# Kernel tuning notes

Hardware: AMD Instinct MI355X
Metric: run time of the kernel (lower is better)

The kernel has to match this reference:

```python
import jax, jax.numpy as jnp
import numpy as np

ROPE_BASE = 10000.0

def _rope_cos_sin(T, d, dtype):
    inv_freq = 1.0 / (ROPE_BASE ** (jnp.arange(0, d, 2, dtype=jnp.float32) / d))
    t = jnp.arange(T, dtype=jnp.float32)
    freqs = t[:, None] * inv_freq[None, :]           # [T, d/2]
    emb = jnp.concatenate([freqs, freqs], axis=-1)   # [T, d]
    return jnp.cos(emb).astype(dtype), jnp.sin(emb).astype(dtype)

def _rotate_half(x):
    x1, x2 = jnp.split(x, 2, axis=-1)
    return jnp.concatenate([-x2, x1], axis=-1)

def setup_inputs() -> dict:
    key = jax.random.key(0)
    k1, k2, k3, k4 = jax.random.split(key, 4)
    B, T, C, H = 4, 4096, 1024, 64
    x = jax.random.normal(k1, (B, T, C), dtype=jnp.float32)
    s = 1.0 / np.sqrt(C)
    Wq = jax.random.normal(k2, (H, C), dtype=jnp.float32) * s
    Wk = jax.random.normal(k3, (H, C), dtype=jnp.float32) * s
    Wv = jax.random.normal(k4, (H, C), dtype=jnp.float32) * s
    return {"x": x, "Wq": Wq, "Wk": Wk, "Wv": Wv}

def reference(x, Wq, Wk, Wv):
    B, T, C = x.shape
    H = Wq.shape[0]
    q = jnp.einsum('btc,hc->bth', x, Wq)
    k = jnp.einsum('btc,hc->bth', x, Wk)
    v = jnp.einsum('btc,hc->bth', x, Wv)
    cos, sin = _rope_cos_sin(T, H, x.dtype)
    q = q * cos + _rotate_half(q) * sin
    k = k * cos + _rotate_half(k) * sin
    # NOTE: original scales by dim_model**-0.5 (C), not head_size
    wei = jnp.einsum('bth,bsh->bts', q, k) * (C ** -0.5)
    causal = jnp.tril(jnp.ones((T, T), dtype=bool))
    wei = jnp.where(causal, wei, -jnp.inf)
    wei = jax.nn.softmax(wei, axis=-1)
    # dropout p=0.0 (identity)
    out = jnp.einsum('bts,bsh->bth', wei, v)
    return out
```

## Files before the change

### kernel.cpp

```cpp
#include <hip/hip_runtime.h>
#include <hip/hip_bf16.h>
#include <math.h>

typedef __attribute__((ext_vector_type(8))) __bf16 bf16x8;
typedef __attribute__((ext_vector_type(4))) float f32x4;
typedef __attribute__((ext_vector_type(16))) float f32x16;
typedef __attribute__((ext_vector_type(4))) float float4_t;
typedef __attribute__((ext_vector_type(4))) unsigned int uint4_t;

#define NB 4
#define TSEQ 4096
#define CD 1024
#define HD 64
#define NCH 16
#define CHT 4
#define QB 32

static __device__ __forceinline__ unsigned short f2bf(float f) {
    union { float f; unsigned u; } v; v.f = f;
    unsigned r = v.u + 0x7fffu + ((v.u >> 16) & 1u);
    return (unsigned short)(r >> 16);
}
static __device__ __forceinline__ float bf2f(unsigned short u) {
    union { unsigned int i; float f; } v; v.i = ((unsigned int)u) << 16;
    return v.f;
}
static __device__ __forceinline__ unsigned int pk2(float a, float b) {
    union { __bf16 h[2]; unsigned int u; } x;
    x.h[0] = (__bf16)a; x.h[1] = (__bf16)b;
    return x.u;
}

__global__ __launch_bounds__(256) void wcvt_kernel(const float* __restrict__ wq,
                                                   const float* __restrict__ wk,
                                                   const float* __restrict__ wv,
                                                   unsigned short* __restrict__ wb) {
    int i = blockIdx.x * 256 + threadIdx.x;
    int j = i >> 10;
    int col = i & 1023;
    int jb = j >> 4, off = j & 15;
    int sub = ((jb & 1) << 5) | ((jb & 2) << 3);
    int srcrow = (jb < 8) ? (sub + off) : ((jb - 8) * 16 + off);
    const float* src = (jb < 4) ? wq : ((jb < 8) ? wk : wv);
    wb[i] = f2bf(src[srcrow * 1024 + col]);
}

__global__ __launch_bounds__(256) void qkv_kernel(const float* __restrict__ x,
                                                  const unsigned short* __restrict__ wb,
                                                  unsigned short* __restrict__ qo,
                                                  unsigned short* __restrict__ ko,
                                                  unsigned short* __restrict__ vt) {
    __shared__ unsigned short xs[64][72];
    __shared__ unsigned short ws[64][72];
    const int tid = threadIdx.x;
    const int wave = tid >> 6, lane = tid & 63;
    const int lr = lane & 15;
    const int lk = (lane >> 4) << 3;
    const int rowg = (lane >> 4) << 2;
    const int row0 = blockIdx.x * 64;
    const int cbi = blockIdx.y;
    const int cb = cbi * 64;

    f32x4 acc[4];
#pragma unroll
    for (int i = 0; i < 4; ++i) acc[i] = (f32x4){0.f, 0.f, 0.f, 0.f};

    const int sr = tid >> 2;
    const int sc = (tid & 3) << 4;

    for (int k0 = 0; k0 < CD; k0 += 64) {
        __syncthreads();
        {
            const float4_t* s4 =
                reinterpret_cast<const float4_t*>(x + (size_t)(row0 + sr) * CD + k0 + sc);
            alignas(16) unsigned short tmp[16];
#pragma unroll
            for (int j = 0; j < 4; ++j) {
                float4_t f = s4[j];
#pragma unroll
                for (int e = 0; e < 4; ++e) tmp[j * 4 + e] = f2bf(f[e]);
            }
            *reinterpret_cast<uint4_t*>(&xs[sr][sc]) = *reinterpret_cast<const uint4_t*>(&tmp[0]);
            *reinterpret_cast<uint4_t*>(&xs[sr][sc + 8]) = *reinterpret_cast<const uint4_t*>(&tmp[8]);
        }
        {
            const uint4_t* wsrc =
                reinterpret_cast<const uint4_t*>(wb + (size_t)(cb + sr) * CD + k0 + sc);
            *reinterpret_cast<uint4_t*>(&ws[sr][sc]) = wsrc[0];
            *reinterpret_cast<uint4_t*>(&ws[sr][sc + 8]) = wsrc[1];
        }
        __syncthreads();
#pragma unroll
        for (int kk = 0; kk < 2; ++kk) {
            bf16x8 a = *reinterpret_cast<const bf16x8*>(&xs[wave * 16 + lr][kk * 32 + lk]);
#pragma unroll
            for (int c = 0; c < 4; ++c) {
                bf16x8 bfr = *reinterpret_cast<const bf16x8*>(&ws[c * 16 + lr][kk * 32 + lk]);
                acc[c] = __builtin_amdgcn_mfma_f32_16x16x32_bf16(a, bfr, acc[c], 0, 0, 0);
            }
        }
    }

    const int gr0 = row0 + wave * 16 + rowg;
    const int bidx = gr0 >> 12;
    const int tb = gr0 & (TSEQ - 1);
    if (cbi < 2) {
        unsigned short* o = (cbi == 0) ? qo : ko;
        const float sc2 = (cbi == 0) ? 0.045084218764560315f : 1.0f;
        const float l2b = 0.4152410118609215f;
        const float invf0 = exp2f(-(float)lr * l2b);
        const float invf1 = exp2f(-(float)(lr + 16) * l2b);
#pragma unroll
        for (int r = 0; r < 4; ++r) {
            float t = (float)(tb + r);
            float s0, c0, s1, c1;
            sincosf(t * invf0, &s0, &c0);
            sincosf(t * invf1, &s1, &c1);
            size_t ro = (size_t)(gr0 + r) * HD;
            float lo, hi;
            lo = acc[0][r]; hi = acc[1][r];
            o[ro + 0 + lr]  = f2bf((lo * c0 - hi * s0) * sc2);
            o[ro + 32 + lr] = f2bf((hi * c0 + lo * s0) * sc2);
            lo = acc[2][r]; hi = acc[3][r];
            o[ro + 16 + lr] = f2bf((lo * c1 - hi * s1) * sc2);
            o[ro + 48 + lr] = f2bf((hi * c1 + lo * s1) * sc2);
        }
    } else {
#pragma unroll
        for (int r = 0; r < 4; ++r) {
            size_t vbase = (size_t)bidx * HD * TSEQ + (size_t)(tb + r);
            vt[vbase + (size_t)(0 + lr) * TSEQ]  = f2bf(acc[0][r]);
            vt[vbase + (size_t)(16 + lr) * TSEQ] = f2bf(acc[1][r]);
            vt[vbase + (size_t)(32 + lr) * TSEQ] = f2bf(acc[2][r]);
            vt[vbase + (size_t)(48 + lr) * TSEQ] = f2bf(acc[3][r]);
        }
    }
}

__global__ __launch_bounds__(256, 4) void attn_partial(const unsigned short* __restrict__ q,
                                                       const unsigned short* __restrict__ k,
                                                       const unsigned short* __restrict__ vt,
                                                       unsigned short* __restrict__ po,
                                                       float* __restrict__ pm,
                                                       float* __restrict__ pl) {
    const int chunk = blockIdx.x, qb = blockIdx.y, b = blockIdx.z;
    const int ktend_blk = 2 * qb + 1;
    const int kt0 = chunk * CHT;
    if (kt0 > ktend_blk) return;
    const int ktend = min(ktend_blk, kt0 + CHT - 1);

    __shared__ unsigned short ks[64][72];
    __shared__ unsigned short vs[64][72];
    const int tid = threadIdx.x;
    const int wave = tid >> 6, lane = tid & 63;
    const int l31 = lane & 31;
    const int h = lane >> 5;
    const int h8 = h << 3;
    const int qrow0 = qb * 128 + wave * 32;
    const int qpos = qrow0 + l31;

    const unsigned short* qb_ = q + ((size_t)(b * TSEQ + qpos)) * HD + h8;
    bf16x8 qf[4];
#pragma unroll
    for (int s = 0; s < 4; ++s)
        qf[s] = *reinterpret_cast<const bf16x8*>(qb_ + 16 * s);

    f32x16 oacc[2];
#pragma unroll
    for (int dt = 0; dt < 2; ++dt)
#pragma unroll
        for (int r = 0; r < 16; ++r) oacc[dt][r] = 0.f;
    float mreg = -1.0e30f;
    float lsum = 0.f;

    const int srow = tid >> 2;
    const int scol = (tid & 3) << 4;
    const unsigned short* kbase = k + (size_t)b * TSEQ * HD;
    const unsigned short* vbase = vt + (size_t)b * HD * TSEQ;
    uint4_t kr[2], vr[2];

    auto loadtile = [&](int kt) {
        const int s0l = kt * 64;
        const unsigned short* kp = kbase + (size_t)(s0l + srow) * HD + scol;
        const unsigned short* vp = vbase + (size_t)srow * TSEQ + s0l + scol;
        kr[0] = *reinterpret_cast<const uint4_t*>(kp);
        kr[1] = *reinterpret_cast<const uint4_t*>(kp + 8);
        vr[0] = *reinterpret_cast<const uint4_t*>(vp);
        vr[1] = *reinterpret_cast<const uint4_t*>(vp + 8);
    };

    loadtile(kt0);

    for (int kt = kt0; kt <= ktend; ++kt) {
        const int s0 = kt * 64;
        __syncthreads();
        *reinterpret_cast<uint4_t*>(&ks[srow][scol]) = kr[0];
        *reinterpret_cast<uint4_t*>(&ks[srow][scol + 8]) = kr[1];
        *reinterpret_cast<uint4_t*>(&vs[srow][scol]) = vr[0];
        *reinterpret_cast<uint4_t*>(&vs[srow][scol + 8]) = vr[1];
        __syncthreads();
        if (kt < ktend) loadtile(kt + 1);

        if (s0 > qrow0 + 31) continue;

        f32x16 sacc[2];
#pragma unroll
        for (int blk = 0; blk < 2; ++blk)
#pragma unroll
            for (int r = 0; r < 16; ++r) sacc[blk][r] = 0.f;
        __builtin_amdgcn_s_setprio(1);
#pragma unroll
        for (int s = 0; s < 4; ++s) {
            bf16x8 ka = *reinterpret_cast<const bf16x8*>(&ks[l31][16 * s + h8]);
            bf16x8 kb2 = *reinterpret_cast<const bf16x8*>(&ks[32 + l31][16 * s + h8]);
            sacc[0] = __builtin_amdgcn_mfma_f32_32x32x16_bf16(ka, qf[s], sacc[0], 0, 0, 0);
            sacc[1] = __builtin_amdgcn_mfma_f32_32x32x16_bf16(kb2, qf[s], sacc[1], 0, 0, 0);
        }
        __builtin_amdgcn_s_setprio(0);

        if (s0 + 63 > qrow0) {
#pragma unroll
            for (int blk = 0; blk < 2; ++blk)
#pragma unroll
                for (int r = 0; r < 16; ++r) {
                    int kvpos = s0 + 32 * blk + (r & 3) + ((r >> 2) << 3) + (h << 2);
                    if (kvpos > qpos) sacc[blk][r] = -INFINITY;
                }
        }

        float tm[8];
#pragma unroll
        for (int r = 0; r < 8; ++r)
            tm[r] = fmaxf(fmaxf(sacc[0][r], sacc[0][r + 8]),
                          fmaxf(sacc[1][r], sacc[1][r + 8]));
#pragma unroll
        for (int r = 0; r < 4; ++r) tm[r] = fmaxf(tm[r], tm[r + 4]);
        float mx = fmaxf(fmaxf(tm[0], tm[1]), fmaxf(tm[2], tm[3]));
        mx = fmaxf(mx, __shfl_xor(mx, 32, 64));

        const bool newmax = !__all(mx <= mreg + 7.0f);
        if (newmax) {
            float mnew = fmaxf(mreg, mx);
            float corr = __builtin_amdgcn_exp2f(mreg - mnew);
            mreg = mnew;
            lsum *= corr;
#pragma unroll
            for (int dt = 0; dt < 2; ++dt)
#pragma unroll
                for (int r = 0; r < 16; ++r) oacc[dt][r] *= corr;
        }

        float pvv[2][16];
#pragma unroll
        for (int blk = 0; blk < 2; ++blk)
#pragma unroll
            for (int r = 0; r < 16; ++r)
                pvv[blk][r] = __builtin_amdgcn_exp2f(sacc[blk][r] - mreg);
        float ts[8];
#pragma unroll
        for (int r = 0; r < 8; ++r)
            ts[r] = (pvv[0][r] + pvv[0][r + 8]) + (pvv[1][r] + pvv[1][r + 8]);
#pragma unroll
        for (int r = 0; r < 4; ++r) ts[r] += ts[r + 4];
        float psum = (ts[0] + ts[1]) + (ts[2] + ts[3]);
        psum += __shfl_xor(psum, 32, 64);
        lsum += psum;

        unsigned int cw[2][4][2];
#pragma unroll
        for (int blk = 0; blk < 2; ++blk)
#pragma unroll
            for (int G = 0; G < 4; ++G) {
                cw[blk][G][0] = pk2(pvv[blk][4 * G], pvv[blk][4 * G + 1]);
                cw[blk][G][1] = pk2(pvv[blk][4 * G + 2], pvv[blk][4 * G + 3]);
            }

        const bool hif = (h == 1);
        __builtin_amdgcn_s_setprio(1);
#pragma unroll
        for (int s = 0; s < 4; ++s) {
            const int blk = s >> 1, base = (s & 1) << 1;
            unsigned int a0 = cw[blk][base][0],     a1 = cw[blk][base][1];
            unsigned int b0 = cw[blk][base + 1][0], b1 = cw[blk][base + 1][1];
            unsigned int s0w = hif ? a0 : b0;
            unsigned int s1w = hif ? a1 : b1;
            unsigned int r0 = __shfl_xor(s0w, 32, 64);
            unsigned int r1 = __shfl_xor(s1w, 32, 64);
            uint4_t pw;
            pw[0] = hif ? r0 : a0;
            pw[1] = hif ? r1 : a1;
            pw[2] = hif ? b0 : r0;
            pw[3] = hif ? b1 : r1;
            bf16x8 pfrag = *reinterpret_cast<const bf16x8*>(&pw);
            bf16x8 v0 = *reinterpret_cast<const bf16x8*>(&vs[l31][16 * s + h8]);
            bf16x8 v1 = *reinterpret_cast<const bf16x8*>(&vs[32 + l31][16 * s + h8]);
            oacc[0] = __builtin_amdgcn_mfma_f32_32x32x16_bf16(v0, pfrag, oacc[0], 0, 0, 0);
            oacc[1] = __builtin_amdgcn_mfma_f32_32x32x16_bf16(v1, pfrag, oacc[1], 0, 0, 0);
        }
        __builtin_amdgcn_s_setprio(0);
    }

    const int slot = (((b << 5) + qb) << 4) + chunk;
    unsigned short* pob = po + (size_t)slot * 8192;
#pragma unroll
    for (int dt = 0; dt < 2; ++dt)
#pragma unroll
        for (int r = 0; r < 16; ++r) {
            int d = 32 * dt + (r & 3) + ((r >> 2) << 3) + (h << 2);
            pob[d * 128 + wave * 32 + l31] = f2bf(oacc[dt][r]);
        }
    if (h == 0) {
        pm[slot * 128 + wave * 32 + l31] = mreg;
        pl[slot * 128 + wave * 32 + l31] = lsum;
    }
}

__global__ __launch_bounds__(256) void attn_combine(const unsigned short* __restrict__ po,
                                                    const float* __restrict__ pm,
                                                    const float* __restrict__ pl,
                                                    float* __restrict__ out) {
    __shared__ float sm[64][17];
    const int bq = blockIdx.x;
    const int dg = blockIdx.y;
    const int qt = bq & 63;
    const int b = bq >> 6;
    const int qb = qt >> 1, half = qt & 1;
    const int nch = (qb >> 1) + 1;
    const int qi = threadIdx.x & 63;
    const int jj = threadIdx.x >> 6;
    const int slotb = (((b << 5) + qb) << 4);
    const int qoff = half * 64 + qi;

    float pmv[NCH];
#pragma unroll
    for (int c = 0; c < NCH; ++c)
        pmv[c] = (c < nch) ? pm[(size_t)(slotb + c) * 128 + qoff] : -1.0e30f;
    float tmv[NCH];
#pragma unroll
    for (int c = 0; c < NCH; ++c) tmv[c] = pmv[c];
#pragma unroll
    for (int s = NCH / 2; s >= 1; s >>= 1)
#pragma unroll
        for (int c = 0; c < NCH / 2; ++c)
            if (c < s) tmv[c] = fmaxf(tmv[c], tmv[c + s]);
    const float M = tmv[0];

    float L = 0.f;
    float a0 = 0.f, a1 = 0.f, a2 = 0.f, a3 = 0.f;
    const int dbase = dg * 16 + jj * 4;
#pragma unroll 4
    for (int c = 0; c < nch; ++c) {
        float w = exp2f(pmv[c] - M);
        L += w * pl[(size_t)(slotb + c) * 128 + qoff];
        const unsigned short* p = po + (size_t)(slotb + c) * 8192 + dbase * 128 + qoff;
        a0 += w * bf2f(p[0]);
        a1 += w * bf2f(p[128]);
        a2 += w * bf2f(p[256]);
        a3 += w * bf2f(p[384]);
    }
    const float inv = 1.f / L;
    sm[qi][jj * 4 + 0] = a0 * inv;
    sm[qi][jj * 4 + 1] = a1 * inv;
    sm[qi][jj * 4 + 2] = a2 * inv;
    sm[qi][jj * 4 + 3] = a3 * inv;
    __syncthreads();
    const int row = threadIdx.x >> 2;
    const int c4 = (threadIdx.x & 3) << 2;
    float4_t f;
#pragma unroll
    for (int e = 0; e < 4; ++e) f[e] = sm[row][c4 + e];
    *reinterpret_cast<float4_t*>(out + (size_t)bq * 4096 + row * 64 + dg * 16 + c4) = f;
}

extern "C" void kernel_launch(void* const* d_in, const int* in_sizes, int n_in,
                              void* d_out, int out_size, void* d_ws, size_t ws_size,
                              hipStream_t stream) {
    const float* x = (const float*)d_in[0];
    const float* wq = (const float*)d_in[1];
    const float* wk = (const float*)d_in[2];
    const float* wv = (const float*)d_in[3];
    float* out = (float*)d_out;

    unsigned short* wb = (unsigned short*)d_ws;
    unsigned short* qb = wb + 3 * HD * CD;
    unsigned short* kb = qb + (size_t)NB * TSEQ * HD;
    unsigned short* vtb = kb + (size_t)NB * TSEQ * HD;
    unsigned short* pob = vtb + (size_t)NB * TSEQ * HD;
    float* pm = (float*)(pob + (size_t)2048 * 8192);
    float* pl = pm + (size_t)2048 * 128;

    wcvt_kernel<<<768, 256, 0, stream>>>(wq, wk, wv, wb);
    qkv_kernel<<<dim3(256, 3), 256, 0, stream>>>(x, wb, qb, kb, vtb);
    attn_partial<<<dim3(NCH, QB, NB), 256, 0, stream>>>(qb, kb, vtb, pob, pm, pl);
    attn_combine<<<dim3(NB * 64, 4), 256, 0, stream>>>(pob, pm, pl, out);
}
```

Baseline: 63.29 us.

## Enlarge attention query block to 256 rows with 512-thread blocks

```diff
diff --git a/kernel.cpp b/kernel.cpp
--- a/kernel.cpp
+++ b/kernel.cpp
@@ -14,7 +14,7 @@
 #define HD 64
 #define NCH 16
 #define CHT 4
-#define QB 32
+#define QBL 16
 
 static __device__ __forceinline__ unsigned short f2bf(float f) {
     union { float f; unsigned u; } v; v.f = f;
@@ -73,15 +73,14 @@
         {
             const float4_t* s4 =
                 reinterpret_cast<const float4_t*>(x + (size_t)(row0 + sr) * CD + k0 + sc);
-            alignas(16) unsigned short tmp[16];
-#pragma unroll
-            for (int j = 0; j < 4; ++j) {
-                float4_t f = s4[j];
-#pragma unroll
-                for (int e = 0; e < 4; ++e) tmp[j * 4 + e] = f2bf(f[e]);
-            }
-            *reinterpret_cast<uint4_t*>(&xs[sr][sc]) = *reinterpret_cast<const uint4_t*>(&tmp[0]);
-            *reinterpret_cast<uint4_t*>(&xs[sr][sc + 8]) = *reinterpret_cast<const uint4_t*>(&tmp[8]);
+            float4_t f0 = s4[0], f1 = s4[1], f2 = s4[2], f3 = s4[3];
+            uint4_t w0, w1;
+            w0[0] = pk2(f0[0], f0[1]); w0[1] = pk2(f0[2], f0[3]);
+            w0[2] = pk2(f1[0], f1[1]); w0[3] = pk2(f1[2], f1[3]);
+            w1[0] = pk2(f2[0], f2[1]); w1[1] = pk2(f2[2], f2[3]);
+            w1[2] = pk2(f3[0], f3[1]); w1[3] = pk2(f3[2], f3[3]);
+            *reinterpret_cast<uint4_t*>(&xs[sr][sc]) = w0;
+            *reinterpret_cast<uint4_t*>(&xs[sr][sc + 8]) = w1;
         }
         {
             const uint4_t* wsrc =
@@ -137,14 +136,14 @@
     }
 }
 
-__global__ __launch_bounds__(256, 4) void attn_partial(const unsigned short* __restrict__ q,
+__global__ __launch_bounds__(512, 4) void attn_partial(const unsigned short* __restrict__ q,
                                                        const unsigned short* __restrict__ k,
                                                        const unsigned short* __restrict__ vt,
                                                        unsigned short* __restrict__ po,
                                                        float* __restrict__ pm,
                                                        float* __restrict__ pl) {
     const int chunk = blockIdx.x, qb = blockIdx.y, b = blockIdx.z;
-    const int ktend_blk = 2 * qb + 1;
+    const int ktend_blk = 4 * qb + 3;
     const int kt0 = chunk * CHT;
     if (kt0 > ktend_blk) return;
     const int ktend = min(ktend_blk, kt0 + CHT - 1);
@@ -156,7 +155,7 @@
     const int l31 = lane & 31;
     const int h = lane >> 5;
     const int h8 = h << 3;
-    const int qrow0 = qb * 128 + wave * 32;
+    const int qrow0 = qb * 256 + wave * 32;
     const int qpos = qrow0 + l31;
 
     const unsigned short* qb_ = q + ((size_t)(b * TSEQ + qpos)) * HD + h8;
@@ -173,20 +172,16 @@
     float mreg = -1.0e30f;
     float lsum = 0.f;
 
-    const int srow = tid >> 2;
-    const int scol = (tid & 3) << 4;
+    const int srow = tid >> 3;
+    const int scol = (tid & 7) << 3;
     const unsigned short* kbase = k + (size_t)b * TSEQ * HD;
     const unsigned short* vbase = vt + (size_t)b * HD * TSEQ;
-    uint4_t kr[2], vr[2];
+    uint4_t kr, vr;
 
     auto loadtile = [&](int kt) {
         const int s0l = kt * 64;
-        const unsigned short* kp = kbase + (size_t)(s0l + srow) * HD + scol;
-        const unsigned short* vp = vbase + (size_t)srow * TSEQ + s0l + scol;
-        kr[0] = *reinterpret_cast<const uint4_t*>(kp);
-        kr[1] = *reinterpret_cast<const uint4_t*>(kp + 8);
-        vr[0] = *reinterpret_cast<const uint4_t*>(vp);
-        vr[1] = *reinterpret_cast<const uint4_t*>(vp + 8);
+        kr = *reinterpret_cast<const uint4_t*>(kbase + (size_t)(s0l + srow) * HD + scol);
+        vr = *reinterpret_cast<const uint4_t*>(vbase + (size_t)srow * TSEQ + s0l + scol);
     };
 
     loadtile(kt0);
@@ -194,10 +189,8 @@
     for (int kt = kt0; kt <= ktend; ++kt) {
         const int s0 = kt * 64;
         __syncthreads();
-        *reinterpret_cast<uint4_t*>(&ks[srow][scol]) = kr[0];
-        *reinterpret_cast<uint4_t*>(&ks[srow][scol + 8]) = kr[1];
-        *reinterpret_cast<uint4_t*>(&vs[srow][scol]) = vr[0];
-        *reinterpret_cast<uint4_t*>(&vs[srow][scol + 8]) = vr[1];
+        *reinterpret_cast<uint4_t*>(&ks[srow][scol]) = kr;
+        *reinterpret_cast<uint4_t*>(&vs[srow][scol]) = vr;
         __syncthreads();
         if (kt < ktend) loadtile(kt + 1);
 
@@ -300,18 +293,18 @@
         __builtin_amdgcn_s_setprio(0);
     }
 
-    const int slot = (((b << 5) + qb) << 4) + chunk;
-    unsigned short* pob = po + (size_t)slot * 8192;
+    const int slot = (((b << 4) + qb) << 4) + chunk;
+    unsigned short* pob = po + (size_t)slot * 16384;
 #pragma unroll
     for (int dt = 0; dt < 2; ++dt)
 #pragma unroll
         for (int r = 0; r < 16; ++r) {
             int d = 32 * dt + (r & 3) + ((r >> 2) << 3) + (h << 2);
-            pob[d * 128 + wave * 32 + l31] = f2bf(oacc[dt][r]);
+            pob[d * 256 + wave * 32 + l31] = f2bf(oacc[dt][r]);
         }
     if (h == 0) {
-        pm[slot * 128 + wave * 32 + l31] = mreg;
-        pl[slot * 128 + wave * 32 + l31] = lsum;
+        pm[slot * 256 + wave * 32 + l31] = mreg;
+        pl[slot * 256 + wave * 32 + l31] = lsum;
     }
 }
 
@@ -324,17 +317,17 @@
     const int dg = blockIdx.y;
     const int qt = bq & 63;
     const int b = bq >> 6;
-    const int qb = qt >> 1, half = qt & 1;
-    const int nch = (qb >> 1) + 1;
+    const int qb = qt >> 2, quarter = qt & 3;
+    const int nch = qb + 1;
     const int qi = threadIdx.x & 63;
     const int jj = threadIdx.x >> 6;
-    const int slotb = (((b << 5) + qb) << 4);
-    const int qoff = half * 64 + qi;
+    const int slotb = (((b << 4) + qb) << 4);
+    const int qoff = quarter * 64 + qi;
 
     float pmv[NCH];
 #pragma unroll
     for (int c = 0; c < NCH; ++c)
-        pmv[c] = (c < nch) ? pm[(size_t)(slotb + c) * 128 + qoff] : -1.0e30f;
+        pmv[c] = (c < nch) ? pm[(size_t)(slotb + c) * 256 + qoff] : -1.0e30f;
     float tmv[NCH];
 #pragma unroll
     for (int c = 0; c < NCH; ++c) tmv[c] = pmv[c];
@@ -351,12 +344,12 @@
 #pragma unroll 4
     for (int c = 0; c < nch; ++c) {
         float w = exp2f(pmv[c] - M);
-        L += w * pl[(size_t)(slotb + c) * 128 + qoff];
-        const unsigned short* p = po + (size_t)(slotb + c) * 8192 + dbase * 128 + qoff;
+        L += w * pl[(size_t)(slotb + c) * 256 + qoff];
+        const unsigned short* p = po + (size_t)(slotb + c) * 16384 + dbase * 256 + qoff;
         a0 += w * bf2f(p[0]);
-        a1 += w * bf2f(p[128]);
-        a2 += w * bf2f(p[256]);
-        a3 += w * bf2f(p[384]);
+        a1 += w * bf2f(p[256]);
+        a2 += w * bf2f(p[512]);
+        a3 += w * bf2f(p[768]);
     }
     const float inv = 1.f / L;
     sm[qi][jj * 4 + 0] = a0 * inv;
@@ -386,11 +379,11 @@
     unsigned short* kb = qb + (size_t)NB * TSEQ * HD;
     unsigned short* vtb = kb + (size_t)NB * TSEQ * HD;
     unsigned short* pob = vtb + (size_t)NB * TSEQ * HD;
-    float* pm = (float*)(pob + (size_t)2048 * 8192);
-    float* pl = pm + (size_t)2048 * 128;
+    float* pm = (float*)(pob + (size_t)1024 * 16384);
+    float* pl = pm + (size_t)1024 * 256;
 
     wcvt_kernel<<<768, 256, 0, stream>>>(wq, wk, wv, wb);
     qkv_kernel<<<dim3(256, 3), 256, 0, stream>>>(x, wb, qb, kb, vtb);
-    attn_partial<<<dim3(NCH, QB, NB), 256, 0, stream>>>(qb, kb, vtb, pob, pm, pl);
+    attn_partial<<<dim3(NCH, QBL, NB), 512, 0, stream>>>(qb, kb, vtb, pob, pm, pl);
     attn_combine<<<dim3(NB * 64, 4), 256, 0, stream>>>(pob, pm, pl, out);
 }
```

New measurement: 63.25 us. About the same (-0.1%).
